# Kernel tuning notes

Measured on AMD Instinct MI355X. Metric: run time of the kernel, lower is better.

## Reference

```python
import jax, jax.numpy as jnp
import numpy as np

NUM_PERTS = 20000
D = 256          # embedding_dim
B, C = 64, 512   # batch_size, num_cells
EPS = 1e-5


def setup_inputs() -> dict:
    key = jax.random.key(0)
    ks = jax.random.split(key, 20)
    inp = {
        'perturbation_ids': jax.random.randint(ks[0], (B, C), 0, NUM_PERTS),
        'table': jax.random.normal(ks[1], (NUM_PERTS, D), dtype=jnp.float32),
    }
    s = 1.0 / np.sqrt(D)
    for i in range(4):
        inp[f'W{i+1}'] = jax.random.uniform(ks[2 + 2 * i], (D, D), minval=-s, maxval=s, dtype=jnp.float32)
        inp[f'b{i+1}'] = jax.random.uniform(ks[3 + 2 * i], (D,), minval=-s, maxval=s, dtype=jnp.float32)
    for i in range(3):
        inp[f'g{i+1}'] = jnp.ones((D,), jnp.float32)
        inp[f'be{i+1}'] = jnp.zeros((D,), jnp.float32)
    return inp


def _bn(x, gamma, beta):
    # BatchNorm1d forward with batch statistics (training-mode math, biased var)
    mu = jnp.mean(x, axis=0)
    var = jnp.mean(jnp.square(x - mu), axis=0)
    return (x - mu) * jax.lax.rsqrt(var + EPS) * gamma + beta


def reference(perturbation_ids, table,
              W1, b1, W2, b2, W3, b3, W4, b4,
              g1, be1, g2, be2, g3, be3):
    # Vectorized replacement of the Python double-loop dict gather
    emb = table[perturbation_ids]                 # (B, C, D)
    x = emb.reshape(-1, D)                        # (B*C, D)
    x = _bn(jax.nn.gelu(x @ W1 + b1, approximate=False), g1, be1)
    x = _bn(jax.nn.gelu(x @ W2 + b2, approximate=False), g2, be2)
    x = _bn(jax.nn.gelu(x @ W3 + b3, approximate=False), g3, be3)
    x = jax.nn.gelu(x @ W4 + b4, approximate=False)
    return x.reshape(B, C, D)
```

## Files before the change

### kernel.cpp

```cpp
#include <hip/hip_runtime.h>
#include <math.h>


typedef __attribute__((ext_vector_type(8))) short short8;
typedef __attribute__((ext_vector_type(4))) float floatx4;

#define NROWS 32768
#define DDIM  256

__device__ __forceinline__ unsigned short f2bf(float f) {
    union { float f; unsigned int u; } v; v.f = f;
    unsigned int r = v.u + 0x7fffu + ((v.u >> 16) & 1u);
    return (unsigned short)(r >> 16);
}

__device__ __forceinline__ float gelu_fast(float x) {
    float z = 0.7978845608f * (x + 0.044715f * x * x * x);
    float e = __expf(2.0f * z);
    float th = 1.0f - 2.0f * __builtin_amdgcn_rcpf(1.0f + e);
    return 0.5f * x * (1.0f + th);
}

__device__ __forceinline__ void load_lds16(const void* g, void* l) {
    __builtin_amdgcn_global_load_lds(
        (__attribute__((address_space(1))) void*)(g),
        (__attribute__((address_space(3))) void*)(l),
        16, 0, 0);
}

__global__ void gather_prep(const int* __restrict__ ids,
                            const float* __restrict__ table,
                            const float* __restrict__ W1,
                            unsigned short* __restrict__ X0,
                            unsigned short* __restrict__ W1t,
                            float* __restrict__ stats )
{
    const int b = blockIdx.x;
    const int t = threadIdx.x;
    if (b < 4096) {
        const int r   = b * 8 + (t >> 5);
        const int lc  = t & 31;
        const int src = ids[r];
        const float4* tp = (const float4*)(table + (size_t)src * DDIM);
        float4 v0 = tp[lc];
        float4 v1 = tp[32 + lc];
        union { unsigned short u[4]; uint2 v; } o0, o1;
        o0.u[0] = f2bf(v0.x); o0.u[1] = f2bf(v0.y);
        o0.u[2] = f2bf(v0.z); o0.u[3] = f2bf(v0.w);
        o1.u[0] = f2bf(v1.x); o1.u[1] = f2bf(v1.y);
        o1.u[2] = f2bf(v1.z); o1.u[3] = f2bf(v1.w);
        *(uint2*)(X0 + (size_t)r * DDIM + lc * 4)       = o0.v;
        *(uint2*)(X0 + (size_t)r * DDIM + 128 + lc * 4) = o1.v;
        if (b == 0) {
            for (int i = t; i < 1536; i += 256) stats[i] = 0.f;
        }
    } else {
        const int n = b - 4096;
        W1t[n * DDIM + t] = f2bf(W1[t * DDIM + n]);
    }
}

template<int WRITE_F32, int DO_STATS>
__global__ __launch_bounds__(256, 2)
void gemm_fused(const unsigned short* __restrict__ A,
                const unsigned short* __restrict__ Bt,
                const float* __restrict__ bias,
                void* __restrict__ outp,
                float* __restrict__ statSum,
                float* __restrict__ statSq)
{
    __shared__ alignas(16) unsigned short As[4096];
    __shared__ alignas(16) unsigned short Bs[4096];
    __shared__ float colsum[128];
    __shared__ float colsq[128];

    const int tid  = threadIdx.x;
    const int wave = tid >> 6;
    const int lane = tid & 63;
    const int quad = lane >> 4;
    const int l15  = lane & 15;
    const int wm   = wave >> 1;
    const int wn   = wave & 1;

    const int m0 = blockIdx.x * 128;
    const int n0 = blockIdx.y * 128;

    const unsigned short* aP0 = A  + (size_t)(m0 +      (tid >> 2)) * DDIM + (tid & 3) * 8;
    const unsigned short* aP1 = A  + (size_t)(m0 + 64 + (tid >> 2)) * DDIM + (tid & 3) * 8;
    const unsigned short* bP0 = Bt + (size_t)(n0 +      (tid >> 2)) * DDIM + (tid & 3) * 8;
    const unsigned short* bP1 = Bt + (size_t)(n0 + 64 + (tid >> 2)) * DDIM + (tid & 3) * 8;
    unsigned short* asD0 = As +        wave * 512;
    unsigned short* asD1 = As + 2048 + wave * 512;
    unsigned short* bsD0 = Bs +        wave * 512;
    unsigned short* bsD1 = Bs + 2048 + wave * 512;

    floatx4 zero = {0.f, 0.f, 0.f, 0.f};
    floatx4 acc[4][4];
#pragma unroll
    for (int i = 0; i < 4; ++i)
#pragma unroll
        for (int j = 0; j < 4; ++j) acc[i][j] = zero;

    float bias_v[4];
#pragma unroll
    for (int nt = 0; nt < 4; ++nt)
        bias_v[nt] = bias[n0 + wn * 64 + nt * 16 + l15];

    for (int kk = 0; kk < 8; ++kk) {
        __syncthreads();
        load_lds16(aP0, asD0);
        load_lds16(aP1, asD1);
        load_lds16(bP0, bsD0);
        load_lds16(bP1, bsD1);
        aP0 += 32; aP1 += 32; bP0 += 32; bP1 += 32;
        __syncthreads();

        short8 af[4], bf[4];
#pragma unroll
        for (int mt = 0; mt < 4; ++mt)
            af[mt] = *(const short8*)(As + (wm * 64 + mt * 16 + l15) * 32 + quad * 8);
#pragma unroll
        for (int nt = 0; nt < 4; ++nt)
            bf[nt] = *(const short8*)(Bs + (wn * 64 + nt * 16 + l15) * 32 + quad * 8);
#pragma unroll
        for (int mt = 0; mt < 4; ++mt)
#pragma unroll
            for (int nt = 0; nt < 4; ++nt)
                acc[mt][nt] = __builtin_amdgcn_mfma_f32_16x16x32_bf16(
                    af[mt], bf[nt], acc[mt][nt], 0, 0, 0);
    }

    float s1[4], s2[4];
#pragma unroll
    for (int nt = 0; nt < 4; ++nt) { s1[nt] = 0.f; s2[nt] = 0.f; }

#pragma unroll
    for (int mt = 0; mt < 4; ++mt) {
        const int rowb = m0 + wm * 64 + mt * 16 + quad * 4;
#pragma unroll
        for (int nt = 0; nt < 4; ++nt) {
            const int col = n0 + wn * 64 + nt * 16 + l15;
#pragma unroll
            for (int i = 0; i < 4; ++i) {
                float y = acc[mt][nt][i] + bias_v[nt];
                y = gelu_fast(y);
                if (WRITE_F32) {
                    ((float*)outp)[(size_t)(rowb + i) * DDIM + col] = y;
                } else {
                    ((unsigned short*)outp)[(size_t)(rowb + i) * DDIM + col] = f2bf(y);
                }
                if (DO_STATS) { s1[nt] += y; s2[nt] += y * y; }
            }
        }
    }

    if (DO_STATS) {
#pragma unroll
        for (int nt = 0; nt < 4; ++nt) {
            s1[nt] += __shfl_xor(s1[nt], 16);
            s1[nt] += __shfl_xor(s1[nt], 32);
            s2[nt] += __shfl_xor(s2[nt], 16);
            s2[nt] += __shfl_xor(s2[nt], 32);
        }
        if (tid < 128) { colsum[tid] = 0.f; colsq[tid] = 0.f; }
        __syncthreads();
        if (quad == 0) {
#pragma unroll
            for (int nt = 0; nt < 4; ++nt) {
                const int c = wn * 64 + nt * 16 + l15;
                atomicAdd(&colsum[c], s1[nt]);
                atomicAdd(&colsq[c], s2[nt]);
            }
        }
        __syncthreads();
        if (tid < 128) {
            atomicAdd(&statSum[n0 + tid], colsum[tid]);
            atomicAdd(&statSq[n0 + tid], colsq[tid]);
        }
    }
}

__global__ void fold_kernel(const float* __restrict__ sum,
                            const float* __restrict__ sq,
                            const float* __restrict__ g,
                            const float* __restrict__ be,
                            const float* __restrict__ W,
                            const float* __restrict__ b,
                            unsigned short* __restrict__ Wt,
                            float* __restrict__ bOut)
{
    __shared__ float sc[256], sh[256], red[4];
    const int t = threadIdx.x;
    const int n = blockIdx.x;
    const float mu  = sum[t] * (1.0f / 32768.0f);
    const float var = sq[t] * (1.0f / 32768.0f) - mu * mu;
    const float scale = rsqrtf(var + 1e-5f) * g[t];
    sc[t] = scale;
    sh[t] = be[t] - mu * scale;
    __syncthreads();
    const float w = W[t * DDIM + n];
    Wt[n * DDIM + t] = f2bf(sc[t] * w);
    float p = sh[t] * w;
#pragma unroll
    for (int o = 32; o; o >>= 1) p += __shfl_down(p, o);
    if ((t & 63) == 0) red[t >> 6] = p;
    __syncthreads();
    if (t == 0) bOut[n] = b[n] + red[0] + red[1] + red[2] + red[3];
}

extern "C" void kernel_launch(void* const* d_in, const int* in_sizes, int n_in,
                              void* d_out, int out_size, void* d_ws, size_t ws_size,
                              hipStream_t stream)
{
    const int*   ids   = (const int*)  d_in[0];
    const float* table = (const float*)d_in[1];
    const float* W[4]  = {(const float*)d_in[2], (const float*)d_in[4],
                          (const float*)d_in[6], (const float*)d_in[8]};
    const float* b[4]  = {(const float*)d_in[3], (const float*)d_in[5],
                          (const float*)d_in[7], (const float*)d_in[9]};
    const float* g[3]  = {(const float*)d_in[10], (const float*)d_in[12], (const float*)d_in[14]};
    const float* be[3] = {(const float*)d_in[11], (const float*)d_in[13], (const float*)d_in[15]};

    unsigned char* ws = (unsigned char*)d_ws;
    unsigned short* buf0 = (unsigned short*)ws;
    unsigned short* buf1 = (unsigned short*)(ws + (size_t)16777216);
    unsigned short* W1t  = (unsigned short*)(ws + (size_t)33554432);
    unsigned short* Wf0  = (unsigned short*)(ws + (size_t)33685504);
    unsigned short* Wf1  = (unsigned short*)(ws + (size_t)33816576);
    unsigned short* Wf2  = (unsigned short*)(ws + (size_t)33947648);
    float* bf0 = (float*)(ws + (size_t)34078720);
    float* bf1 = (float*)(ws + (size_t)34079744);
    float* bf2 = (float*)(ws + (size_t)34080768);
    float* stats = (float*)(ws + (size_t)34081792);
    float *sum0 = stats,        *sq0 = stats + 256;
    float *sum1 = stats + 512,  *sq1 = stats + 768;
    float *sum2 = stats + 1024, *sq2 = stats + 1280;

    gather_prep<<<4352, 256, 0, stream>>>(ids, table, W[0], buf0, W1t, stats);

    dim3 ggrid(256, 2);
    gemm_fused<0, 1><<<ggrid, 256, 0, stream>>>(buf0, W1t, b[0], buf1, sum0, sq0);
    fold_kernel<<<256, 256, 0, stream>>>(sum0, sq0, g[0], be[0], W[1], b[1], Wf0, bf0);
    gemm_fused<0, 1><<<ggrid, 256, 0, stream>>>(buf1, Wf0, bf0, buf0, sum1, sq1);
    fold_kernel<<<256, 256, 0, stream>>>(sum1, sq1, g[1], be[1], W[2], b[2], Wf1, bf1);
    gemm_fused<0, 1><<<ggrid, 256, 0, stream>>>(buf0, Wf1, bf1, buf1, sum2, sq2);
    fold_kernel<<<256, 256, 0, stream>>>(sum2, sq2, g[2], be[2], W[3], b[3], Wf2, bf2);
    gemm_fused<1, 0><<<ggrid, 256, 0, stream>>>(buf1, Wf2, bf2, (void*)d_out, nullptr, nullptr);
}
```

Measured before the change: 191.8 us.

## Fuse whole encoder into one cooperative persistent kernel with grid syncs

Replaces the eight-launch pipeline (gather, four GEMMs, three weight folds) with a single cooperative kernel of 512 blocks. Each block keeps its 64-row activation tile resident in LDS across all four layers and uses grid-wide syncs for the BatchNorm statistics. BN is applied in place on the LDS tile rather than folded into the next weights. This removes launch overhead and the global round trips of intermediate activations, at the cost of grid-sync latency and the requirement that all 512 blocks be co-resident, with the old multi-kernel path kept as a fallback if the cooperative launch fails.

```diff
diff --git a/kernel.cpp b/kernel.cpp
--- a/kernel.cpp
+++ b/kernel.cpp
@@ -1,26 +1,30 @@
 #include <hip/hip_runtime.h>
+#include <hip/hip_cooperative_groups.h>
 #include <math.h>
+
+namespace cg = cooperative_groups;
 
 
 typedef __attribute__((ext_vector_type(8))) short short8;
 typedef __attribute__((ext_vector_type(4))) float floatx4;
 
-#define NROWS 32768
-#define DDIM  256
+#define DDIM 256
 
 __device__ __forceinline__ unsigned short f2bf(float f) {
     union { float f; unsigned int u; } v; v.f = f;
     unsigned int r = v.u + 0x7fffu + ((v.u >> 16) & 1u);
     return (unsigned short)(r >> 16);
 }
-
+__device__ __forceinline__ float bf2f(unsigned short u) {
+    union { unsigned int i; float f; } v; v.i = ((unsigned int)u) << 16;
+    return v.f;
+}
 __device__ __forceinline__ float gelu_fast(float x) {
     float z = 0.7978845608f * (x + 0.044715f * x * x * x);
     float e = __expf(2.0f * z);
     float th = 1.0f - 2.0f * __builtin_amdgcn_rcpf(1.0f + e);
     return 0.5f * x * (1.0f + th);
 }
-
 __device__ __forceinline__ void load_lds16(const void* g, void* l) {
     __builtin_amdgcn_global_load_lds(
         (__attribute__((address_space(1))) void*)(g),
@@ -28,12 +32,187 @@
         16, 0, 0);
 }
 
+
+struct Params {
+    const int* ids; const float* table;
+    const float* W[4]; const float* b[4];
+    const float* g[3]; const float* be[3];
+    unsigned short* Wt;
+    float* stats;
+    float* out;
+};
+
+__global__ __launch_bounds__(256, 2) void fused_encoder(Params p)
+{
+    __shared__ alignas(16) unsigned short Albs[64 * 256];
+    __shared__ alignas(16) unsigned short Wlds[16384];
+    cg::grid_group grid = cg::this_grid();
+
+    const int tid  = threadIdx.x;
+    const int blk  = blockIdx.x;
+    const int wave = tid >> 6;
+    const int lane = tid & 63;
+    const int quad = lane >> 4;
+    const int l15  = lane & 15;
+    const int wn   = wave;
+    const int row0 = blk * 64;
+
+    for (int it = 0; it < 8; ++it) {
+        const int r   = it * 8 + (tid >> 5);
+        const int g   = tid & 31;
+        const int src = p.ids[row0 + r];
+        const float4* tp = (const float4*)(p.table + (size_t)src * 256 + g * 8);
+        float4 v0 = tp[0], v1 = tp[1];
+        union { unsigned short u[8]; uint4 v; } o;
+        o.u[0]=f2bf(v0.x); o.u[1]=f2bf(v0.y); o.u[2]=f2bf(v0.z); o.u[3]=f2bf(v0.w);
+        o.u[4]=f2bf(v1.x); o.u[5]=f2bf(v1.y); o.u[6]=f2bf(v1.z); o.u[7]=f2bf(v1.w);
+        *(uint4*)(Albs + r * 256 + (g ^ (r & 7)) * 8) = o.v;
+    }
+    {
+        const int j  = blk >> 7;
+        const int c0 = (blk & 127) * 2;
+        const float* Wj = p.W[j];
+        unsigned short* WtJ = p.Wt + ((size_t)j << 16);
+        WtJ[(size_t)(c0    ) * 256 + tid] = f2bf(Wj[(size_t)tid * 256 + c0    ]);
+        WtJ[(size_t)(c0 + 1) * 256 + tid] = f2bf(Wj[(size_t)tid * 256 + c0 + 1]);
+    }
+    if (blk < 12) {
+        float* s = p.stats + blk * 1024;
+        s[tid] = 0.f; s[tid + 256] = 0.f; s[tid + 512] = 0.f; s[tid + 768] = 0.f;
+    }
+    grid.sync();
+
+    for (int layer = 0; layer < 4; ++layer) {
+        __syncthreads();
+
+        const unsigned short* WtL = p.Wt + ((size_t)layer << 16);
+        float bias_v[4];
+#pragma unroll
+        for (int nt = 0; nt < 4; ++nt)
+            bias_v[nt] = p.b[layer][wn * 64 + nt * 16 + l15];
+
+        floatx4 acc[4][4];
+#pragma unroll
+        for (int i = 0; i < 4; ++i)
+#pragma unroll
+            for (int j = 0; j < 4; ++j)
+                acc[i][j] = floatx4{0.f, 0.f, 0.f, 0.f};
+
+        auto stage = [&](int kk, int hb) {
+            const int q = ((lane & 3) ^ ((lane >> 3) & 3)) * 8;
+            const unsigned short* gs = WtL
+                + (size_t)(wn * 64 + (lane >> 2)) * 256 + kk * 32 + q;
+            unsigned short* ld = Wlds + wn * 4096 + hb * 2048;
+            load_lds16(gs,            ld);
+            load_lds16(gs + 16 * 256, ld + 512);
+            load_lds16(gs + 32 * 256, ld + 1024);
+            load_lds16(gs + 48 * 256, ld + 1536);
+        };
+
+        stage(0, 0);
+        for (int kk = 0; kk < 8; ++kk) {
+            const int hb = kk & 1;
+            if (kk < 7) {
+                stage(kk + 1, hb ^ 1);
+                __builtin_amdgcn_s_waitcnt(0x0F74);
+            } else {
+                __builtin_amdgcn_s_waitcnt(0x0F70);
+            }
+            short8 af[4], bfr[4];
+            const int agp   = ((kk * 4 + quad) ^ (l15 & 7)) * 8;
+            const int bslot = (quad ^ ((l15 >> 1) & 3)) * 8;
+#pragma unroll
+            for (int mt = 0; mt < 4; ++mt)
+                af[mt] = *(const short8*)(Albs + (mt * 16 + l15) * 256 + agp);
+#pragma unroll
+            for (int nt = 0; nt < 4; ++nt)
+                bfr[nt] = *(const short8*)(Wlds + wn * 4096 + hb * 2048
+                                           + (nt * 16 + l15) * 32 + bslot);
+#pragma unroll
+            for (int mt = 0; mt < 4; ++mt)
+#pragma unroll
+                for (int nt = 0; nt < 4; ++nt)
+                    acc[mt][nt] = __builtin_amdgcn_mfma_f32_16x16x32_bf16(
+                        af[mt], bfr[nt], acc[mt][nt], 0, 0, 0);
+        }
+
+        if (layer < 3) {
+            __syncthreads();
+            float s1[4] = {0.f, 0.f, 0.f, 0.f};
+            float s2[4] = {0.f, 0.f, 0.f, 0.f};
+#pragma unroll
+            for (int mt = 0; mt < 4; ++mt) {
+#pragma unroll
+                for (int nt = 0; nt < 4; ++nt) {
+                    const int col = wn * 64 + nt * 16 + l15;
+#pragma unroll
+                    for (int i = 0; i < 4; ++i) {
+                        const int row = mt * 16 + quad * 4 + i;
+                        float y = gelu_fast(acc[mt][nt][i] + bias_v[nt]);
+                        Albs[row * 256 + ((col >> 3) ^ (row & 7)) * 8 + (col & 7)]
+                            = f2bf(y);
+                        s1[nt] += y; s2[nt] += y * y;
+                    }
+                }
+            }
+#pragma unroll
+            for (int nt = 0; nt < 4; ++nt) {
+                s1[nt] += __shfl_xor(s1[nt], 16); s1[nt] += __shfl_xor(s1[nt], 32);
+                s2[nt] += __shfl_xor(s2[nt], 16); s2[nt] += __shfl_xor(s2[nt], 32);
+            }
+            float* sb = p.stats + layer * 4096 + (blk & 7) * 512;
+            if (quad == 0) {
+#pragma unroll
+                for (int nt = 0; nt < 4; ++nt) {
+                    const int col = wn * 64 + nt * 16 + l15;
+                    atomicAdd(&sb[col],       s1[nt]);
+                    atomicAdd(&sb[256 + col], s2[nt]);
+                }
+            }
+            grid.sync();
+
+            {
+                const float* st = p.stats + layer * 4096;
+                float sum = 0.f, sq = 0.f;
+#pragma unroll
+                for (int s = 0; s < 8; ++s) {
+                    sum += st[s * 512 + tid];
+                    sq  += st[s * 512 + 256 + tid];
+                }
+                const float mu  = sum * (1.f / 32768.f);
+                const float var = sq * (1.f / 32768.f) - mu * mu;
+                const float scl = rsqrtf(var + 1e-5f) * p.g[layer][tid];
+                const float shf = p.be[layer][tid] - mu * scl;
+                const int gt = tid >> 3, ct = tid & 7;
+                for (int r = 0; r < 64; ++r) {
+                    const int idx = r * 256 + ((gt ^ (r & 7)) * 8) + ct;
+                    Albs[idx] = f2bf(fmaf(bf2f(Albs[idx]), scl, shf));
+                }
+            }
+        } else {
+#pragma unroll
+            for (int mt = 0; mt < 4; ++mt) {
+                const int rb = row0 + mt * 16 + quad * 4;
+#pragma unroll
+                for (int nt = 0; nt < 4; ++nt) {
+                    const int col = wn * 64 + nt * 16 + l15;
+#pragma unroll
+                    for (int i = 0; i < 4; ++i)
+                        p.out[(size_t)(rb + i) * 256 + col] =
+                            gelu_fast(acc[mt][nt][i] + bias_v[nt]);
+                }
+            }
+        }
+    }
+}
+
+
 __global__ void gather_prep(const int* __restrict__ ids,
                             const float* __restrict__ table,
                             const float* __restrict__ W1,
                             unsigned short* __restrict__ X0,
                             unsigned short* __restrict__ W1t,
-                            float* __restrict__ stats )
+                            float* __restrict__ stats)
 {
     const int b = blockIdx.x;
     const int t = threadIdx.x;
@@ -200,10 +379,10 @@
     __syncthreads();
     const float w = W[t * DDIM + n];
     Wt[n * DDIM + t] = f2bf(sc[t] * w);
-    float p = sh[t] * w;
-#pragma unroll
-    for (int o = 32; o; o >>= 1) p += __shfl_down(p, o);
-    if ((t & 63) == 0) red[t >> 6] = p;
+    float pp = sh[t] * w;
+#pragma unroll
+    for (int o = 32; o; o >>= 1) pp += __shfl_down(pp, o);
+    if ((t & 63) == 0) red[t >> 6] = pp;
     __syncthreads();
     if (t == 0) bOut[n] = b[n] + red[0] + red[1] + red[2] + red[3];
 }
@@ -214,36 +393,53 @@
 {
     const int*   ids   = (const int*)  d_in[0];
     const float* table = (const float*)d_in[1];
-    const float* W[4]  = {(const float*)d_in[2], (const float*)d_in[4],
-                          (const float*)d_in[6], (const float*)d_in[8]};
-    const float* b[4]  = {(const float*)d_in[3], (const float*)d_in[5],
-                          (const float*)d_in[7], (const float*)d_in[9]};
-    const float* g[3]  = {(const float*)d_in[10], (const float*)d_in[12], (const float*)d_in[14]};
-    const float* be[3] = {(const float*)d_in[11], (const float*)d_in[13], (const float*)d_in[15]};
+
+    Params prm;
+    prm.ids   = ids;
+    prm.table = table;
+    prm.W[0] = (const float*)d_in[2];  prm.b[0] = (const float*)d_in[3];
+    prm.W[1] = (const float*)d_in[4];  prm.b[1] = (const float*)d_in[5];
+    prm.W[2] = (const float*)d_in[6];  prm.b[2] = (const float*)d_in[7];
+    prm.W[3] = (const float*)d_in[8];  prm.b[3] = (const float*)d_in[9];
+    prm.g[0]  = (const float*)d_in[10]; prm.be[0] = (const float*)d_in[11];
+    prm.g[1]  = (const float*)d_in[12]; prm.be[1] = (const float*)d_in[13];
+    prm.g[2]  = (const float*)d_in[14]; prm.be[2] = (const float*)d_in[15];
 
     unsigned char* ws = (unsigned char*)d_ws;
-    unsigned short* buf0 = (unsigned short*)ws;
-    unsigned short* buf1 = (unsigned short*)(ws + (size_t)16777216);
-    unsigned short* W1t  = (unsigned short*)(ws + (size_t)33554432);
-    unsigned short* Wf0  = (unsigned short*)(ws + (size_t)33685504);
-    unsigned short* Wf1  = (unsigned short*)(ws + (size_t)33816576);
-    unsigned short* Wf2  = (unsigned short*)(ws + (size_t)33947648);
-    float* bf0 = (float*)(ws + (size_t)34078720);
-    float* bf1 = (float*)(ws + (size_t)34079744);
-    float* bf2 = (float*)(ws + (size_t)34080768);
-    float* stats = (float*)(ws + (size_t)34081792);
+    prm.Wt    = (unsigned short*)ws;
+    prm.stats = (float*)(ws + (size_t)524288);
+    prm.out   = (float*)d_out;
+
+    void* args[] = { &prm };
+    hipError_t cerr = hipLaunchCooperativeKernel((const void*)fused_encoder,
+                                                 dim3(512), dim3(256), args,
+                                                 0, stream);
+    if (cerr == hipSuccess) return;
+
+    unsigned short* buf0 = (unsigned short*)(ws + (size_t)1048576);
+    unsigned short* buf1 = (unsigned short*)(ws + (size_t)1048576 + 16777216);
+    unsigned short* W1t  = (unsigned short*)(ws + (size_t)1048576 + 33554432);
+    unsigned short* Wf0  = (unsigned short*)(ws + (size_t)1048576 + 33685504);
+    unsigned short* Wf1  = (unsigned short*)(ws + (size_t)1048576 + 33816576);
+    unsigned short* Wf2  = (unsigned short*)(ws + (size_t)1048576 + 33947648);
+    float* bf0 = (float*)(ws + (size_t)1048576 + 34078720);
+    float* bf1 = (float*)(ws + (size_t)1048576 + 34079744);
+    float* bf2 = (float*)(ws + (size_t)1048576 + 34080768);
+    float* stats = (float*)(ws + (size_t)1048576 + 34081792);
     float *sum0 = stats,        *sq0 = stats + 256;
     float *sum1 = stats + 512,  *sq1 = stats + 768;
     float *sum2 = stats + 1024, *sq2 = stats + 1280;
 
-    gather_prep<<<4352, 256, 0, stream>>>(ids, table, W[0], buf0, W1t, stats);
+    const float* W1 = prm.W[0];
+
+    gather_prep<<<4352, 256, 0, stream>>>(ids, table, W1, buf0, W1t, stats);
 
     dim3 ggrid(256, 2);
-    gemm_fused<0, 1><<<ggrid, 256, 0, stream>>>(buf0, W1t, b[0], buf1, sum0, sq0);
-    fold_kernel<<<256, 256, 0, stream>>>(sum0, sq0, g[0], be[0], W[1], b[1], Wf0, bf0);
+    gemm_fused<0, 1><<<ggrid, 256, 0, stream>>>(buf0, W1t, prm.b[0], buf1, sum0, sq0);
+    fold_kernel<<<256, 256, 0, stream>>>(sum0, sq0, prm.g[0], prm.be[0], prm.W[1], prm.b[1], Wf0, bf0);
     gemm_fused<0, 1><<<ggrid, 256, 0, stream>>>(buf1, Wf0, bf0, buf0, sum1, sq1);
-    fold_kernel<<<256, 256, 0, stream>>>(sum1, sq1, g[1], be[1], W[2], b[2], Wf1, bf1);
+    fold_kernel<<<256, 256, 0, stream>>>(sum1, sq1, prm.g[1], prm.be[1], prm.W[2], prm.b[2], Wf1, bf1);
     gemm_fused<0, 1><<<ggrid, 256, 0, stream>>>(buf0, Wf1, bf1, buf1, sum2, sq2);
-    fold_kernel<<<256, 256, 0, stream>>>(sum2, sq2, g[2], be[2], W[3], b[3], Wf2, bf2);
+    fold_kernel<<<256, 256, 0, stream>>>(sum2, sq2, prm.g[2], prm.be[2], prm.W[3], prm.b[3], Wf2, bf2);
     gemm_fused<1, 0><<<ggrid, 256, 0, stream>>>(buf1, Wf2, bf2, (void*)d_out, nullptr, nullptr);
 }
```

Measured after the change: 380.9 us. 98.6% more time.

## Fuse embedding gather into first GEMM and restructure GEMM to full-K LDS tiles

Applied to the files above, without the earlier changes.

The separate gather/convert pass is removed: the first GEMM gathers table rows by id, converts them to bf16 and writes them into a swizzled LDS tile. Each block now handles 64 rows by all 256 columns, with the whole K=256 A tile loaded once, and the weight fragments read directly from global memory instead of staged through LDS. The per-k-step syncs go away, and BN statistics are accumulated with global atomics into 8 shards that the fold kernel sums. The trade-off is uncached global weight reads per wave, 32KB of LDS per block, and fewer, larger blocks.

```diff
diff --git a/kernel.cpp b/kernel.cpp
--- a/kernel.cpp
+++ b/kernel.cpp
@@ -5,15 +5,13 @@
 typedef __attribute__((ext_vector_type(8))) short short8;
 typedef __attribute__((ext_vector_type(4))) float floatx4;
 
-#define NROWS 32768
-#define DDIM  256
+#define DDIM 256
 
 __device__ __forceinline__ unsigned short f2bf(float f) {
     union { float f; unsigned int u; } v; v.f = f;
     unsigned int r = v.u + 0x7fffu + ((v.u >> 16) & 1u);
     return (unsigned short)(r >> 16);
 }
-
 __device__ __forceinline__ float gelu_fast(float x) {
     float z = 0.7978845608f * (x + 0.044715f * x * x * x);
     float e = __expf(2.0f * z);
@@ -21,167 +19,139 @@
     return 0.5f * x * (1.0f + th);
 }
 
-__device__ __forceinline__ void load_lds16(const void* g, void* l) {
-    __builtin_amdgcn_global_load_lds(
-        (__attribute__((address_space(1))) void*)(g),
-        (__attribute__((address_space(3))) void*)(l),
-        16, 0, 0);
-}
-
-__global__ void gather_prep(const int* __restrict__ ids,
-                            const float* __restrict__ table,
-                            const float* __restrict__ W1,
-                            unsigned short* __restrict__ X0,
+__global__ void prep_kernel(const float* __restrict__ W1,
                             unsigned short* __restrict__ W1t,
                             float* __restrict__ stats )
 {
-    const int b = blockIdx.x;
-    const int t = threadIdx.x;
-    if (b < 4096) {
-        const int r   = b * 8 + (t >> 5);
-        const int lc  = t & 31;
-        const int src = ids[r];
-        const float4* tp = (const float4*)(table + (size_t)src * DDIM);
-        float4 v0 = tp[lc];
-        float4 v1 = tp[32 + lc];
-        union { unsigned short u[4]; uint2 v; } o0, o1;
-        o0.u[0] = f2bf(v0.x); o0.u[1] = f2bf(v0.y);
-        o0.u[2] = f2bf(v0.z); o0.u[3] = f2bf(v0.w);
-        o1.u[0] = f2bf(v1.x); o1.u[1] = f2bf(v1.y);
-        o1.u[2] = f2bf(v1.z); o1.u[3] = f2bf(v1.w);
-        *(uint2*)(X0 + (size_t)r * DDIM + lc * 4)       = o0.v;
-        *(uint2*)(X0 + (size_t)r * DDIM + 128 + lc * 4) = o1.v;
-        if (b == 0) {
-            for (int i = t; i < 1536; i += 256) stats[i] = 0.f;
-        }
-    } else {
-        const int n = b - 4096;
-        W1t[n * DDIM + t] = f2bf(W1[t * DDIM + n]);
-    }
-}
-
-template<int WRITE_F32, int DO_STATS>
+    const int t = threadIdx.x, b = blockIdx.x;
+    W1t[(size_t)t * DDIM + b] = f2bf(W1[(size_t)b * DDIM + t]);
+    if (b < 12) {
+        float* s = stats + b * 1024;
+        s[t] = 0.f; s[t + 256] = 0.f; s[t + 512] = 0.f; s[t + 768] = 0.f;
+    }
+}
+
+template<int GATHER, int WRITE_F32, int DO_STATS>
 __global__ __launch_bounds__(256, 2)
-void gemm_fused(const unsigned short* __restrict__ A,
-                const unsigned short* __restrict__ Bt,
-                const float* __restrict__ bias,
-                void* __restrict__ outp,
-                float* __restrict__ statSum,
-                float* __restrict__ statSq)
-{
-    __shared__ alignas(16) unsigned short As[4096];
-    __shared__ alignas(16) unsigned short Bs[4096];
-    __shared__ float colsum[128];
-    __shared__ float colsq[128];
+void gemm_enc(const unsigned short* __restrict__ A,
+              const int* __restrict__ ids,
+              const float* __restrict__ table,
+              const unsigned short* __restrict__ Wt,
+              const float* __restrict__ bias,
+              void* __restrict__ outp,
+              float* __restrict__ statShards )
+{
+    __shared__ alignas(16) unsigned short Albs[64 * 256];
 
     const int tid  = threadIdx.x;
+    const int blk  = blockIdx.x;
     const int wave = tid >> 6;
     const int lane = tid & 63;
     const int quad = lane >> 4;
     const int l15  = lane & 15;
-    const int wm   = wave >> 1;
-    const int wn   = wave & 1;
-
-    const int m0 = blockIdx.x * 128;
-    const int n0 = blockIdx.y * 128;
-
-    const unsigned short* aP0 = A  + (size_t)(m0 +      (tid >> 2)) * DDIM + (tid & 3) * 8;
-    const unsigned short* aP1 = A  + (size_t)(m0 + 64 + (tid >> 2)) * DDIM + (tid & 3) * 8;
-    const unsigned short* bP0 = Bt + (size_t)(n0 +      (tid >> 2)) * DDIM + (tid & 3) * 8;
-    const unsigned short* bP1 = Bt + (size_t)(n0 + 64 + (tid >> 2)) * DDIM + (tid & 3) * 8;
-    unsigned short* asD0 = As +        wave * 512;
-    unsigned short* asD1 = As + 2048 + wave * 512;
-    unsigned short* bsD0 = Bs +        wave * 512;
-    unsigned short* bsD1 = Bs + 2048 + wave * 512;
-
-    floatx4 zero = {0.f, 0.f, 0.f, 0.f};
+    const int wn   = wave;
+    const int row0 = blk * 64;
+
+    {
+        const int r  = tid >> 2;
+        const int c0 = (tid & 3) * 64;
+        if (GATHER) {
+            const int src = ids[row0 + r];
+            const float* tp = table + (size_t)src * DDIM + c0;
+#pragma unroll
+            for (int j = 0; j < 8; ++j) {
+                float4 v0 = *(const float4*)(tp + j * 8);
+                float4 v1 = *(const float4*)(tp + j * 8 + 4);
+                union { unsigned short u[8]; uint4 v; } o;
+                o.u[0]=f2bf(v0.x); o.u[1]=f2bf(v0.y); o.u[2]=f2bf(v0.z); o.u[3]=f2bf(v0.w);
+                o.u[4]=f2bf(v1.x); o.u[5]=f2bf(v1.y); o.u[6]=f2bf(v1.z); o.u[7]=f2bf(v1.w);
+                const int g = (tid & 3) * 8 + j;
+                *(uint4*)(Albs + r * 256 + (g ^ (r & 7)) * 8) = o.v;
+            }
+        } else {
+            const unsigned short* ap = A + (size_t)(row0 + r) * DDIM + c0;
+#pragma unroll
+            for (int j = 0; j < 8; ++j) {
+                uint4 v = *(const uint4*)(ap + j * 8);
+                const int g = (tid & 3) * 8 + j;
+                *(uint4*)(Albs + r * 256 + (g ^ (r & 7)) * 8) = v;
+            }
+        }
+    }
+
+    float bias_v[4];
+#pragma unroll
+    for (int nt = 0; nt < 4; ++nt)
+        bias_v[nt] = bias[wn * 64 + nt * 16 + l15];
+
     floatx4 acc[4][4];
 #pragma unroll
     for (int i = 0; i < 4; ++i)
 #pragma unroll
-        for (int j = 0; j < 4; ++j) acc[i][j] = zero;
-
-    float bias_v[4];
-#pragma unroll
-    for (int nt = 0; nt < 4; ++nt)
-        bias_v[nt] = bias[n0 + wn * 64 + nt * 16 + l15];
-
+        for (int j = 0; j < 4; ++j)
+            acc[i][j] = floatx4{0.f, 0.f, 0.f, 0.f};
+
+    __syncthreads();
+
+    const unsigned short* wb = Wt + (size_t)(wn * 64 + l15) * DDIM + quad * 8;
+#pragma unroll 2
     for (int kk = 0; kk < 8; ++kk) {
-        __syncthreads();
-        load_lds16(aP0, asD0);
-        load_lds16(aP1, asD1);
-        load_lds16(bP0, bsD0);
-        load_lds16(bP1, bsD1);
-        aP0 += 32; aP1 += 32; bP0 += 32; bP1 += 32;
-        __syncthreads();
-
-        short8 af[4], bf[4];
+        short8 bfr[4];
+#pragma unroll
+        for (int nt = 0; nt < 4; ++nt)
+            bfr[nt] = *(const short8*)(wb + (size_t)(nt * 16) * DDIM + kk * 32);
+        short8 af[4];
+        const int agp = ((kk * 4 + quad) ^ (l15 & 7)) * 8;
 #pragma unroll
         for (int mt = 0; mt < 4; ++mt)
-            af[mt] = *(const short8*)(As + (wm * 64 + mt * 16 + l15) * 32 + quad * 8);
-#pragma unroll
-        for (int nt = 0; nt < 4; ++nt)
-            bf[nt] = *(const short8*)(Bs + (wn * 64 + nt * 16 + l15) * 32 + quad * 8);
+            af[mt] = *(const short8*)(Albs + (mt * 16 + l15) * 256 + agp);
 #pragma unroll
         for (int mt = 0; mt < 4; ++mt)
 #pragma unroll
             for (int nt = 0; nt < 4; ++nt)
                 acc[mt][nt] = __builtin_amdgcn_mfma_f32_16x16x32_bf16(
-                    af[mt], bf[nt], acc[mt][nt], 0, 0, 0);
-    }
-
-    float s1[4], s2[4];
-#pragma unroll
-    for (int nt = 0; nt < 4; ++nt) { s1[nt] = 0.f; s2[nt] = 0.f; }
-
+                    af[mt], bfr[nt], acc[mt][nt], 0, 0, 0);
+    }
+
+    float s1[4] = {0.f, 0.f, 0.f, 0.f};
+    float s2[4] = {0.f, 0.f, 0.f, 0.f};
 #pragma unroll
     for (int mt = 0; mt < 4; ++mt) {
-        const int rowb = m0 + wm * 64 + mt * 16 + quad * 4;
+        const int rb = row0 + mt * 16 + quad * 4;
 #pragma unroll
         for (int nt = 0; nt < 4; ++nt) {
-            const int col = n0 + wn * 64 + nt * 16 + l15;
+            const int col = wn * 64 + nt * 16 + l15;
 #pragma unroll
             for (int i = 0; i < 4; ++i) {
-                float y = acc[mt][nt][i] + bias_v[nt];
-                y = gelu_fast(y);
+                float y = gelu_fast(acc[mt][nt][i] + bias_v[nt]);
                 if (WRITE_F32) {
-                    ((float*)outp)[(size_t)(rowb + i) * DDIM + col] = y;
+                    ((float*)outp)[(size_t)(rb + i) * DDIM + col] = y;
                 } else {
-                    ((unsigned short*)outp)[(size_t)(rowb + i) * DDIM + col] = f2bf(y);
+                    ((unsigned short*)outp)[(size_t)(rb + i) * DDIM + col] = f2bf(y);
                 }
                 if (DO_STATS) { s1[nt] += y; s2[nt] += y * y; }
             }
         }
     }
-
     if (DO_STATS) {
 #pragma unroll
         for (int nt = 0; nt < 4; ++nt) {
-            s1[nt] += __shfl_xor(s1[nt], 16);
-            s1[nt] += __shfl_xor(s1[nt], 32);
-            s2[nt] += __shfl_xor(s2[nt], 16);
-            s2[nt] += __shfl_xor(s2[nt], 32);
-        }
-        if (tid < 128) { colsum[tid] = 0.f; colsq[tid] = 0.f; }
-        __syncthreads();
+            s1[nt] += __shfl_xor(s1[nt], 16); s1[nt] += __shfl_xor(s1[nt], 32);
+            s2[nt] += __shfl_xor(s2[nt], 16); s2[nt] += __shfl_xor(s2[nt], 32);
+        }
+        float* sb = statShards + (blk & 7) * 512;
         if (quad == 0) {
 #pragma unroll
             for (int nt = 0; nt < 4; ++nt) {
-                const int c = wn * 64 + nt * 16 + l15;
-                atomicAdd(&colsum[c], s1[nt]);
-                atomicAdd(&colsq[c], s2[nt]);
-            }
-        }
-        __syncthreads();
-        if (tid < 128) {
-            atomicAdd(&statSum[n0 + tid], colsum[tid]);
-            atomicAdd(&statSq[n0 + tid], colsq[tid]);
-        }
-    }
-}
-
-__global__ void fold_kernel(const float* __restrict__ sum,
-                            const float* __restrict__ sq,
+                const int col = wn * 64 + nt * 16 + l15;
+                atomicAdd(&sb[col],       s1[nt]);
+                atomicAdd(&sb[256 + col], s2[nt]);
+            }
+        }
+    }
+}
+
+__global__ void fold_kernel(const float* __restrict__ shards,
                             const float* __restrict__ g,
                             const float* __restrict__ be,
                             const float* __restrict__ W,
@@ -192,18 +162,24 @@
     __shared__ float sc[256], sh[256], red[4];
     const int t = threadIdx.x;
     const int n = blockIdx.x;
-    const float mu  = sum[t] * (1.0f / 32768.0f);
-    const float var = sq[t] * (1.0f / 32768.0f) - mu * mu;
+    float sum = 0.f, sq = 0.f;
+#pragma unroll
+    for (int s = 0; s < 8; ++s) {
+        sum += shards[s * 512 + t];
+        sq  += shards[s * 512 + 256 + t];
+    }
+    const float mu  = sum * (1.0f / 32768.0f);
+    const float var = sq * (1.0f / 32768.0f) - mu * mu;
     const float scale = rsqrtf(var + 1e-5f) * g[t];
     sc[t] = scale;
     sh[t] = be[t] - mu * scale;
     __syncthreads();
     const float w = W[t * DDIM + n];
     Wt[n * DDIM + t] = f2bf(sc[t] * w);
-    float p = sh[t] * w;
-#pragma unroll
-    for (int o = 32; o; o >>= 1) p += __shfl_down(p, o);
-    if ((t & 63) == 0) red[t >> 6] = p;
+    float pp = sh[t] * w;
+#pragma unroll
+    for (int o = 32; o; o >>= 1) pp += __shfl_down(pp, o);
+    if ((t & 63) == 0) red[t >> 6] = pp;
     __syncthreads();
     if (t == 0) bOut[n] = b[n] + red[0] + red[1] + red[2] + red[3];
 }
@@ -214,36 +190,40 @@
 {
     const int*   ids   = (const int*)  d_in[0];
     const float* table = (const float*)d_in[1];
-    const float* W[4]  = {(const float*)d_in[2], (const float*)d_in[4],
-                          (const float*)d_in[6], (const float*)d_in[8]};
-    const float* b[4]  = {(const float*)d_in[3], (const float*)d_in[5],
-                          (const float*)d_in[7], (const float*)d_in[9]};
-    const float* g[3]  = {(const float*)d_in[10], (const float*)d_in[12], (const float*)d_in[14]};
-    const float* be[3] = {(const float*)d_in[11], (const float*)d_in[13], (const float*)d_in[15]};
+    const float* W1 = (const float*)d_in[2];  const float* b1 = (const float*)d_in[3];
+    const float* W2 = (const float*)d_in[4];  const float* b2 = (const float*)d_in[5];
+    const float* W3 = (const float*)d_in[6];  const float* b3 = (const float*)d_in[7];
+    const float* W4 = (const float*)d_in[8];  const float* b4 = (const float*)d_in[9];
+    const float* g1 = (const float*)d_in[10]; const float* be1 = (const float*)d_in[11];
+    const float* g2 = (const float*)d_in[12]; const float* be2 = (const float*)d_in[13];
+    const float* g3 = (const float*)d_in[14]; const float* be3 = (const float*)d_in[15];
 
     unsigned char* ws = (unsigned char*)d_ws;
-    unsigned short* buf0 = (unsigned short*)ws;
-    unsigned short* buf1 = (unsigned short*)(ws + (size_t)16777216);
-    unsigned short* W1t  = (unsigned short*)(ws + (size_t)33554432);
-    unsigned short* Wf0  = (unsigned short*)(ws + (size_t)33685504);
-    unsigned short* Wf1  = (unsigned short*)(ws + (size_t)33816576);
-    unsigned short* Wf2  = (unsigned short*)(ws + (size_t)33947648);
-    float* bf0 = (float*)(ws + (size_t)34078720);
-    float* bf1 = (float*)(ws + (size_t)34079744);
-    float* bf2 = (float*)(ws + (size_t)34080768);
-    float* stats = (float*)(ws + (size_t)34081792);
-    float *sum0 = stats,        *sq0 = stats + 256;
-    float *sum1 = stats + 512,  *sq1 = stats + 768;
-    float *sum2 = stats + 1024, *sq2 = stats + 1280;
-
-    gather_prep<<<4352, 256, 0, stream>>>(ids, table, W[0], buf0, W1t, stats);
-
-    dim3 ggrid(256, 2);
-    gemm_fused<0, 1><<<ggrid, 256, 0, stream>>>(buf0, W1t, b[0], buf1, sum0, sq0);
-    fold_kernel<<<256, 256, 0, stream>>>(sum0, sq0, g[0], be[0], W[1], b[1], Wf0, bf0);
-    gemm_fused<0, 1><<<ggrid, 256, 0, stream>>>(buf1, Wf0, bf0, buf0, sum1, sq1);
-    fold_kernel<<<256, 256, 0, stream>>>(sum1, sq1, g[1], be[1], W[2], b[2], Wf1, bf1);
-    gemm_fused<0, 1><<<ggrid, 256, 0, stream>>>(buf0, Wf1, bf1, buf1, sum2, sq2);
-    fold_kernel<<<256, 256, 0, stream>>>(sum2, sq2, g[2], be[2], W[3], b[3], Wf2, bf2);
-    gemm_fused<1, 0><<<ggrid, 256, 0, stream>>>(buf1, Wf2, bf2, (void*)d_out, nullptr, nullptr);
-}
+    unsigned short* W1t = (unsigned short*)ws;
+    unsigned short* W2t = (unsigned short*)(ws + (size_t)131072);
+    unsigned short* W3t = (unsigned short*)(ws + (size_t)262144);
+    unsigned short* W4t = (unsigned short*)(ws + (size_t)393216);
+    float* bb2   = (float*)(ws + (size_t)524288);
+    float* bb3   = (float*)(ws + (size_t)525312);
+    float* bb4   = (float*)(ws + (size_t)526336);
+    float* stats = (float*)(ws + (size_t)527360);
+    unsigned short* act1 = (unsigned short*)(ws + (size_t)1048576);
+    unsigned short* act2 = (unsigned short*)(ws + (size_t)17825792);
+
+    prep_kernel<<<256, 256, 0, stream>>>(W1, W1t, stats);
+
+    gemm_enc<1, 0, 1><<<512, 256, 0, stream>>>(nullptr, ids, table, W1t, b1,
+                                               act1, stats);
+    fold_kernel<<<256, 256, 0, stream>>>(stats, g1, be1, W2, b2, W2t, bb2);
+
+    gemm_enc<0, 0, 1><<<512, 256, 0, stream>>>(act1, nullptr, nullptr, W2t, bb2,
+                                               act2, stats + 4096);
+    fold_kernel<<<256, 256, 0, stream>>>(stats + 4096, g2, be2, W3, b3, W3t, bb3);
+
+    gemm_enc<0, 0, 1><<<512, 256, 0, stream>>>(act2, nullptr, nullptr, W3t, bb3,
+                                               act1, stats + 8192);
+    fold_kernel<<<256, 256, 0, stream>>>(stats + 8192, g3, be3, W4, b4, W4t, bb4);
+
+    gemm_enc<0, 1, 0><<<512, 256, 0, stream>>>(act1, nullptr, nullptr, W4t, bb4,
+                                               (void*)d_out, nullptr);
+}
```

Result: faster. 182.2 us (-5.0%).
